# Kernel tuning notes

Measured on AMD Instinct MI355X. Metric: run time of the kernel, lower is better.

Reference implementation:

```python
import jax, jax.numpy as jnp
import numpy as np

NEG = -1e30  # stands in for -inf on the diagonal; exp(NEG - max) == 0 exactly


def setup_inputs() -> dict:
    key = jax.random.key(0)
    k1, k2, k3, k4, k5 = jax.random.split(key, 5)
    B, C, H, W = 4, 512, 128, 128
    mid = C // 8  # 64
    x = jax.random.normal(k1, (B, C, H, W), dtype=jnp.float32)
    Wq = jax.random.normal(k2, (mid, C), dtype=jnp.float32) * (1.0 / np.sqrt(C))
    Wk = jax.random.normal(k3, (mid, C), dtype=jnp.float32) * (1.0 / np.sqrt(C))
    Wv = jax.random.normal(k4, (C, C), dtype=jnp.float32) * (1.0 / np.sqrt(C))
    gamma = jax.random.normal(k5, (1,), dtype=jnp.float32) * 0.1
    return {"x": x, "Wq": Wq, "Wk": Wk, "Wv": Wv, "gamma": gamma}


def reference(x, Wq, Wk, Wv, gamma):
    B, C, H, W = x.shape
    # 1x1 convs == channel matmuls
    q = jnp.einsum('bchw,mc->bmhw', x, Wq)  # (B, mid, H, W)
    k = jnp.einsum('bchw,mc->bmhw', x, Wk)
    v = jnp.einsum('bchw,dc->bdhw', x, Wv)  # (B, C, H, W)

    # vertical (H-axis) logits with -inf diagonal: eH[b,i,w,j] = sum_m q[b,m,i,w] k[b,m,j,w]
    eH = jnp.einsum('bmiw,bmjw->biwj', q, k)           # (B, H, W, H)
    diag = jnp.eye(H, dtype=bool)[:, None, :]          # (H, 1, H)
    eH = jnp.where(diag, NEG, eH)

    # horizontal (W-axis) logits: eW[b,h,i,j] = sum_m q[b,m,h,i] k[b,m,h,j]
    eW = jnp.einsum('bmhi,bmhj->bhij', q, k)           # (B, H, W, W)

    # joint softmax over the concatenated H+W logits
    attn = jax.nn.softmax(jnp.concatenate([eH, eW], axis=3), axis=3)  # (B, H, W, H+W)
    aH = attn[:, :, :, :H]  # (B, H, W, H)
    aW = attn[:, :, :, H:]  # (B, H, W, W)

    # attention-weighted value aggregation along each axis
    outH = jnp.einsum('bcjw,biwj->bciw', v, aH)  # (B, C, H, W)
    outW = jnp.einsum('bchj,bhij->bchi', v, aW)  # (B, C, H, W)

    return gamma[0] * (outH + outW) + x
```

## Files before the change

kernel.cpp:

```cpp
#include <hip/hip_runtime.h>
#include <cstdint>
#include <cstddef>

#define NEGV (-1e30f)

constexpr int C_ = 512, H_ = 128, W_ = 128;
constexpr int P_ = 16384;

typedef short bf16x8 __attribute__((ext_vector_type(8)));
typedef float f32x4  __attribute__((ext_vector_type(4)));
typedef _Float16 f16x4 __attribute__((ext_vector_type(4)));
#define MFMA16(a, b, c) __builtin_amdgcn_mfma_f32_16x16x32_bf16((a), (b), (c), 0, 0, 0)

#define SWZ128(r, cs) (((r) << 7) + (((((cs) >> 3) ^ ((r) & 7))) << 3) + ((cs) & 7))
#define SWZ64(r, cs)  (((r) << 6) + (((((cs) >> 3) ^ ((r) & 7))) << 3) + ((cs) & 7))

__device__ inline void gl_lds16(const void* g, void* l) {
    __builtin_amdgcn_global_load_lds(
        (const __attribute__((address_space(1))) unsigned int*)g,
        (__attribute__((address_space(3))) unsigned int*)l, 16, 0, 0);
}

__device__ inline unsigned short f2bf(float f) {
    union { float f; uint32_t i; } t; t.f = f;
    uint32_t r = t.i + 0x7FFFu + ((t.i >> 16) & 1u);
    return (unsigned short)(r >> 16);
}

__global__ __launch_bounds__(256) void kwconv(
    const float* __restrict__ Wq, const float* __restrict__ Wk,
    const float* __restrict__ Wv,
    unsigned short* __restrict__ Wqkbf, unsigned short* __restrict__ Wvbf)
{
    const int i4 = (blockIdx.x * 256 + threadIdx.x) * 4;
    const float* src; unsigned short* dst; int off;
    if (i4 < 32768)       { src = Wq + i4;          dst = Wqkbf + i4; }
    else if (i4 < 65536)  { off = i4 - 32768; src = Wk + off; dst = Wqkbf + i4; }
    else                  { off = i4 - 65536; src = Wv + off; dst = Wvbf + off; }
    const float4 v = *(const float4*)src;
    ushort4 u; u.x = f2bf(v.x); u.y = f2bf(v.y); u.z = f2bf(v.z); u.w = f2bf(v.w);
    *(ushort4*)dst = u;
}

__global__ __launch_bounds__(256) void kprep1(
    const float* __restrict__ x, unsigned short* __restrict__ xTbf,
    unsigned short* __restrict__ xbf)
{
    __shared__ float t[32][33];
    const int tid = threadIdx.x;
    const int h0 = (blockIdx.x >> 2) * 32, w0 = (blockIdx.x & 3) * 32;
    const size_t base = (size_t)blockIdx.y * P_;
    {
        const int r = tid >> 3, c4 = (tid & 7) * 4;
        const float4 v = *(const float4*)&x[base + (size_t)(h0 + r) * 128 + w0 + c4];
        t[r][c4] = v.x; t[r][c4 + 1] = v.y; t[r][c4 + 2] = v.z; t[r][c4 + 3] = v.w;
        if (xbf) {
            ushort4 u; u.x = f2bf(v.x); u.y = f2bf(v.y); u.z = f2bf(v.z); u.w = f2bf(v.w);
            *(ushort4*)&xbf[base + (size_t)(h0 + r) * 128 + w0 + c4] = u;
        }
    }
    __syncthreads();
    {
        const int wr = tid >> 3, hc = (tid & 7) * 4;
        ushort4 u;
        u.x = f2bf(t[hc][wr]);     u.y = f2bf(t[hc + 1][wr]);
        u.z = f2bf(t[hc + 2][wr]); u.w = f2bf(t[hc + 3][wr]);
        *(ushort4*)&xTbf[base + (size_t)(w0 + wr) * 128 + h0 + hc] = u;
    }
}

__global__ __launch_bounds__(256) void kprep2(
    const float* __restrict__ x, unsigned short* __restrict__ xbfT)
{
    __shared__ float t[32][33];
    const int tid = threadIdx.x;
    const int p0 = blockIdx.x * 32, c0 = blockIdx.y * 32, b = blockIdx.z;
    {
        const int r = tid >> 3, c4 = (tid & 7) * 4;
        const float4 v = *(const float4*)&x[((size_t)(b * C_ + c0 + r)) * P_ + p0 + c4];
        t[r][c4] = v.x; t[r][c4 + 1] = v.y; t[r][c4 + 2] = v.z; t[r][c4 + 3] = v.w;
    }
    __syncthreads();
    {
        const int pr = tid >> 3, cc = (tid & 7) * 4;
        ushort4 u;
        u.x = f2bf(t[cc][pr]);     u.y = f2bf(t[cc + 1][pr]);
        u.z = f2bf(t[cc + 2][pr]); u.w = f2bf(t[cc + 3][pr]);
        *(ushort4*)&xbfT[((size_t)b * P_ + p0 + pr) * C_ + c0 + cc] = u;
    }
}

__global__ __launch_bounds__(256) void kgemmqk(
    const unsigned short* __restrict__ A, const unsigned short* __restrict__ Bm,
    unsigned short* __restrict__ outbf)
{
    __shared__ __attribute__((aligned(16))) unsigned short sA[2][128 * 64];
    __shared__ __attribute__((aligned(16))) unsigned short sB[2][128 * 64];
    const int tid = threadIdx.x;
    const int pbase = blockIdx.x * 128, b = blockIdx.z;
    const int lane = tid & 63, wv = tid >> 6;
    const int m0 = (wv >> 1) * 64, p0 = (wv & 1) * 64;
    const int fr = lane & 15, fq = lane >> 4;

    f32x4 acc[4][4];
#pragma unroll
    for (int i = 0; i < 4; i++)
#pragma unroll
        for (int j = 0; j < 4; j++) acc[i][j] = (f32x4){0.f, 0.f, 0.f, 0.f};

    const size_t brow0 = ((size_t)b * P_ + pbase) * 512;

#define QK_STAGE(chunk, buf) {                                                  \
        const int kc_ = (chunk) * 64;                                           \
        _Pragma("unroll")                                                       \
        for (int rep = 0; rep < 4; rep++) {                                     \
            const int idx = rep * 256 + tid;                                    \
            const int r_ = idx >> 3, kgs = (idx & 7) ^ (r_ & 7);                \
            gl_lds16(&A[(size_t)r_ * 512 + kc_ + kgs * 8], &sA[buf][idx * 8]);  \
            gl_lds16(&Bm[brow0 + (size_t)r_ * 512 + kc_ + kgs * 8], &sB[buf][idx * 8]); \
        } }

    QK_STAGE(0, 0);
    int cur = 0;
    for (int chunk = 0; chunk < 8; ++chunk) {
        if (chunk < 7) {
            QK_STAGE(chunk + 1, cur ^ 1);
            asm volatile("s_waitcnt vmcnt(8)" ::: "memory");
        } else {
            asm volatile("s_waitcnt vmcnt(0)" ::: "memory");
        }
        __builtin_amdgcn_s_barrier();
#pragma unroll
        for (int kk = 0; kk < 64; kk += 32) {
            bf16x8 af[4], bfv[4];
#pragma unroll
            for (int t = 0; t < 4; t++) af[t]  = *(const bf16x8*)&sA[cur][SWZ64(m0 + t * 16 + fr, kk + fq * 8)];
#pragma unroll
            for (int t = 0; t < 4; t++) bfv[t] = *(const bf16x8*)&sB[cur][SWZ64(p0 + t * 16 + fr, kk + fq * 8)];
#pragma unroll
            for (int i = 0; i < 4; i++)
#pragma unroll
                for (int j = 0; j < 4; j++)
                    acc[i][j] = MFMA16(af[i], bfv[j], acc[i][j]);
        }
        if (chunk < 7) __builtin_amdgcn_s_barrier();
        cur ^= 1;
    }
#undef QK_STAGE

#pragma unroll
    for (int tj = 0; tj < 4; tj++) {
        const int p_g = pbase + p0 + tj * 16 + fr;
        const size_t rowo = ((size_t)b * P_ + p_g) * 128;
#pragma unroll
        for (int ti = 0; ti < 4; ti++) {
            const int mk = m0 + ti * 16 + fq * 4;
            ushort4 u;
            u.x = f2bf(acc[ti][tj][0]); u.y = f2bf(acc[ti][tj][1]);
            u.z = f2bf(acc[ti][tj][2]); u.w = f2bf(acc[ti][tj][3]);
            *(ushort4*)&outbf[rowo + mk] = u;
        }
    }
}

__global__ __launch_bounds__(256) void klogits(
    const unsigned short* __restrict__ qkP,
    _Float16* __restrict__ ERow, _Float16* __restrict__ ECol)
{
    __shared__ __attribute__((aligned(16))) unsigned short sPM[128 * 136];
    const int tid = threadIdx.x;
    const int s = blockIdx.x, b = blockIdx.y, mode = blockIdx.z;
    const int rowMul  = mode ? 1 : 128;
    const int rowStep = mode ? 128 : 1;
    _Float16* E = mode ? ECol : ERow;
    const size_t qbase = (size_t)b * P_ * 128;
    const int rb = s * rowMul;
#pragma unroll
    for (int rep = 0; rep < 8; rep++) {
        const int idx = rep * 256 + tid;
        const int mkg = idx & 15, i = idx >> 4;
        *(uint4*)&sPM[i * 136 + mkg * 8] =
            *(const uint4*)&qkP[qbase + (size_t)(rb + i * rowStep) * 128 + mkg * 8];
    }
    __syncthreads();

    const int lane = tid & 63, wv = tid >> 6;
    const int i0 = (wv >> 1) * 64, j0 = (wv & 1) * 64;
    const int fr = lane & 15, fq = lane >> 4;

    f32x4 acc[4][4];
#pragma unroll
    for (int i = 0; i < 4; i++)
#pragma unroll
        for (int j = 0; j < 4; j++) acc[i][j] = (f32x4){0.f, 0.f, 0.f, 0.f};

#pragma unroll
    for (int kk = 0; kk < 64; kk += 32) {
        bf16x8 af[4], bfv[4];
#pragma unroll
        for (int t = 0; t < 4; t++) af[t]  = *(const bf16x8*)&sPM[(i0 + t * 16 + fr) * 136 + kk + fq * 8];
#pragma unroll
        for (int t = 0; t < 4; t++) bfv[t] = *(const bf16x8*)&sPM[(j0 + t * 16 + fr) * 136 + 64 + kk + fq * 8];
#pragma unroll
        for (int i = 0; i < 4; i++)
#pragma unroll
            for (int j = 0; j < 4; j++)
                acc[i][j] = MFMA16(af[i], bfv[j], acc[i][j]);
    }

    _Float16* Eb = E + ((size_t)(b * 128 + s)) * P_;
#pragma unroll
    for (int ti = 0; ti < 4; ti++)
#pragma unroll
        for (int r = 0; r < 4; r++) {
            const int i_g = i0 + ti * 16 + fq * 4 + r;
#pragma unroll
            for (int tj = 0; tj < 4; tj++) {
                const int j_g = j0 + tj * 16 + fr;
                float v = acc[ti][tj][r];
                if (mode && i_g == j_g) v = -60000.0f;
                Eb[(size_t)i_g * 128 + j_g] = (_Float16)v;
            }
        }
}

__global__ __launch_bounds__(256) void ksoftmax(
    const _Float16* __restrict__ ER, const _Float16* __restrict__ EC,
    unsigned short* __restrict__ AR, unsigned short* __restrict__ AC)
{
    const int tid = threadIdx.x;
    const int l32 = tid & 31;
    const int pix = blockIdx.x * 8 + (tid >> 5);
    const int b = pix >> 14, rem = pix & 16383;
    const int h = rem >> 7, w = rem & 127;
    const size_t ro = ((size_t)((b * 128 + h) * 128 + w)) * 128;
    const size_t co = ((size_t)((b * 128 + w) * 128 + h)) * 128;
    const f16x4 r = *(const f16x4*)(ER + ro + l32 * 4);
    const f16x4 c = *(const f16x4*)(EC + co + l32 * 4);
    const float r0 = r.x, r1 = r.y, r2 = r.z, r3 = r.w;
    const float c0 = c.x, c1 = c.y, c2 = c.z, c3 = c.w;
    float mx = fmaxf(fmaxf(fmaxf(r0, r1), fmaxf(r2, r3)),
                     fmaxf(fmaxf(c0, c1), fmaxf(c2, c3)));
#pragma unroll
    for (int off = 16; off > 0; off >>= 1) mx = fmaxf(mx, __shfl_xor(mx, off));
    const float e0 = __expf(r0 - mx), e1 = __expf(r1 - mx);
    const float e2 = __expf(r2 - mx), e3 = __expf(r3 - mx);
    const float f0 = __expf(c0 - mx), f1 = __expf(c1 - mx);
    const float f2 = __expf(c2 - mx), f3 = __expf(c3 - mx);
    float sm = (e0 + e1 + e2 + e3) + (f0 + f1 + f2 + f3);
#pragma unroll
    for (int off = 16; off > 0; off >>= 1) sm += __shfl_xor(sm, off);
    const float inv = 1.0f / sm;
    ushort4 u0, u1;
    u0.x = f2bf(e0 * inv); u0.y = f2bf(e1 * inv); u0.z = f2bf(e2 * inv); u0.w = f2bf(e3 * inv);
    u1.x = f2bf(f0 * inv); u1.y = f2bf(f1 * inv); u1.z = f2bf(f2 * inv); u1.w = f2bf(f3 * inv);
    *(ushort4*)(AR + ro + l32 * 4) = u0;
    *(ushort4*)(AC + co + l32 * 4) = u1;
}

__global__ __launch_bounds__(256) void kagg2(
    const unsigned short* __restrict__ ARow, const unsigned short* __restrict__ ACol,
    const float* __restrict__ x, const unsigned short* __restrict__ xbf,
    const unsigned short* __restrict__ xTbf,
    unsigned short* __restrict__ ySumR, unsigned short* __restrict__ ySumC)
{
    __shared__ __attribute__((aligned(16))) unsigned short sAttn[128 * 128];
    __shared__ __attribute__((aligned(16))) unsigned short sX[128 * 128];
    const int tid = threadIdx.x;
    const int s = blockIdx.x, b = blockIdx.y, mode = blockIdx.z;
    const int lane = tid & 63, wv = tid >> 6;
    const int m0 = (wv >> 1) * 64, n0 = (wv & 1) * 64;
    const int fr = lane & 15, fq = lane >> 4;

    const unsigned short* At = (mode ? ACol : ARow) + ((size_t)(b * 128 + s)) * P_;
#pragma unroll
    for (int rep = 0; rep < 8; rep++) {
        const int idx = rep * 256 + tid;
        const int r = idx >> 4, sl = idx & 15;
        gl_lds16(&At[(size_t)r * 128 + (sl ^ (r & 7)) * 8], &sAttn[idx * 8]);
    }

    unsigned short* yS = mode ? ySumC : ySumR;
    const unsigned short* Xsrc = mode ? xTbf : xbf;

    for (int ct = 0; ct < 4; ct++) {
        if (Xsrc) {
            const unsigned short* Xs = &Xsrc[((size_t)(b * C_ + ct * 128)) * P_ + s * 128];
#pragma unroll
            for (int rep = 0; rep < 8; rep++) {
                const int idx = rep * 256 + tid;
                const int r = idx >> 4, sl = idx & 15;
                gl_lds16(&Xs[(size_t)r * P_ + (sl ^ (r & 7)) * 8], &sX[idx * 8]);
            }
        } else {
            const float* Xf = &x[((size_t)(b * C_ + ct * 128)) * P_ + s * 128];
#pragma unroll
            for (int rep = 0; rep < 16; rep++) {
                const int idx = rep * 256 + tid;
                const int jq = idx & 31, cc = idx >> 5;
                const float4 v = *(const float4*)&Xf[(size_t)cc * P_ + jq * 4];
                ushort4 u; u.x = f2bf(v.x); u.y = f2bf(v.y); u.z = f2bf(v.z); u.w = f2bf(v.w);
                *(ushort4*)&sX[SWZ128(cc, jq * 4)] = u;
            }
        }
        __syncthreads();

        f32x4 acc[4][4];
#pragma unroll
        for (int i = 0; i < 4; i++)
#pragma unroll
            for (int j = 0; j < 4; j++) acc[i][j] = (f32x4){0.f, 0.f, 0.f, 0.f};

#pragma unroll
        for (int kk = 0; kk < 128; kk += 32) {
            bf16x8 af[4], bfv[4];
#pragma unroll
            for (int t = 0; t < 4; t++) {
                const int rc = m0 + t * 16 + fr;
                af[t] = *(const bf16x8*)&sX[SWZ128(rc, kk + fq * 8)];
            }
#pragma unroll
            for (int t = 0; t < 4; t++) {
                const int ri = n0 + t * 16 + fr;
                bfv[t] = *(const bf16x8*)&sAttn[SWZ128(ri, kk + fq * 8)];
            }
#pragma unroll
            for (int i = 0; i < 4; i++)
#pragma unroll
                for (int j = 0; j < 4; j++)
                    acc[i][j] = MFMA16(af[i], bfv[j], acc[i][j]);
        }

        const int cg0 = ct * 128 + m0 + fq * 4;
#pragma unroll
        for (int tj = 0; tj < 4; tj++) {
            const int i_g = n0 + tj * 16 + fr;
            const size_t p = mode ? ((size_t)i_g * 128 + s) : ((size_t)s * 128 + i_g);
            unsigned short* rowp = yS + ((size_t)b * P_ + p) * 512;
#pragma unroll
            for (int ti = 0; ti < 4; ti++) {
                ushort4 u;
                u.x = f2bf(acc[ti][tj][0]); u.y = f2bf(acc[ti][tj][1]);
                u.z = f2bf(acc[ti][tj][2]); u.w = f2bf(acc[ti][tj][3]);
                *(ushort4*)&rowp[cg0 + ti * 16] = u;
            }
        }
        __syncthreads();
    }
}

__global__ __launch_bounds__(512) void kfinalM(
    const unsigned short* __restrict__ Wvbf,
    const unsigned short* __restrict__ yR,
    const unsigned short* __restrict__ yC,
    float* __restrict__ outf,
    const float* __restrict__ addx,
    const float* __restrict__ gammap)
{
    __shared__ __attribute__((aligned(16))) unsigned short sM[512 * 64];
    __shared__ __attribute__((aligned(16))) unsigned short sP[128 * 64];
    const int tid = threadIdx.x;
    const int pbase = blockIdx.x * 128, b = blockIdx.z;
    const int lane = tid & 63, wv = tid >> 6;
    const int m0w = (wv >> 1) * 128;
    const int p0w = (wv & 1) * 64;
    const int fr = lane & 15, fq = lane >> 4;

    f32x4 acc[4][8];
#pragma unroll
    for (int i = 0; i < 4; i++)
#pragma unroll
        for (int j = 0; j < 8; j++) acc[i][j] = (f32x4){0.f, 0.f, 0.f, 0.f};

    const size_t brow = ((size_t)b * P_ + pbase) * 512;

    for (int hc = 0; hc < 16; ++hc) {
        const int kc = (hc >> 1) * 64;
        const unsigned short* Bsrc = (hc & 1) ? yC : yR;
        if (!(hc & 1)) {
#pragma unroll
            for (int rep = 0; rep < 8; rep++) {
                const int idx = rep * 512 + tid;
                const int r_ = idx >> 3, kgs = (idx & 7) ^ (r_ & 7);
                gl_lds16(&Wvbf[(size_t)r_ * 512 + kc + kgs * 8], &sM[idx * 8]);
            }
        }
#pragma unroll
        for (int rep = 0; rep < 2; rep++) {
            const int idx = rep * 512 + tid;
            const int r_ = idx >> 3, kgs = (idx & 7) ^ (r_ & 7);
            gl_lds16(&Bsrc[brow + (size_t)r_ * 512 + kc + kgs * 8], &sP[idx * 8]);
        }
        __syncthreads();
#pragma unroll
        for (int kk = 0; kk < 64; kk += 32) {
            bf16x8 bp[4], am[8];
#pragma unroll
            for (int t = 0; t < 4; t++) bp[t] = *(const bf16x8*)&sP[SWZ64(p0w + t * 16 + fr, kk + fq * 8)];
#pragma unroll
            for (int t = 0; t < 8; t++) am[t] = *(const bf16x8*)&sM[SWZ64(m0w + t * 16 + fr, kk + fq * 8)];
            __builtin_amdgcn_s_setprio(1);
#pragma unroll
            for (int i = 0; i < 4; i++)
#pragma unroll
                for (int j = 0; j < 8; j++)
                    acc[i][j] = MFMA16(bp[i], am[j], acc[i][j]);
            __builtin_amdgcn_s_setprio(0);
        }
        __syncthreads();
    }

    const float g = gammap[0];
#pragma unroll
    for (int ti = 0; ti < 4; ti++) {
        const int p_g = pbase + p0w + ti * 16 + fq * 4;
#pragma unroll
        for (int tj = 0; tj < 8; tj++) {
            const int m_g = m0w + tj * 16 + fr;
            const size_t off = ((size_t)(b * 512 + m_g)) * P_ + p_g;
            const float4 xa = *(const float4*)&addx[off];
            float4 o;
            o.x = fmaf(g, acc[ti][tj][0], xa.x);
            o.y = fmaf(g, acc[ti][tj][1], xa.y);
            o.z = fmaf(g, acc[ti][tj][2], xa.z);
            o.w = fmaf(g, acc[ti][tj][3], xa.w);
            *(float4*)&outf[off] = o;
        }
    }
}

extern "C" void kernel_launch(void* const* d_in, const int* in_sizes, int n_in,
                              void* d_out, int out_size, void* d_ws, size_t ws_size,
                              hipStream_t stream) {
    const float* x     = (const float*)d_in[0];
    const float* Wq    = (const float*)d_in[1];
    const float* Wk    = (const float*)d_in[2];
    const float* Wv    = (const float*)d_in[3];
    const float* gamma = (const float*)d_in[4];
    float* out = (float*)d_out;

    char* base = (char*)d_ws;
    unsigned short* Wqkbf = (unsigned short*)base;             base += 131072;
    unsigned short* Wvbf  = (unsigned short*)base;             base += 524288;
    unsigned short* xTbf  = (unsigned short*)base;             base += 67108864;
    unsigned short* xbfT  = (unsigned short*)base;             base += 67108864;
    unsigned short* qkP   = (unsigned short*)base;             base += 16777216;
    _Float16*       ERow  = (_Float16*)base;                   base += 33554432;
    _Float16*       ECol  = (_Float16*)base;                   base += 33554432;
    unsigned short* ARow  = (unsigned short*)base;             base += 16777216;
    unsigned short* ACol  = (unsigned short*)base;             base += 16777216;
    unsigned short* ySumR = (unsigned short*)base;             base += 67108864;
    unsigned short* ySumC = (unsigned short*)ERow;
    const size_t used = (size_t)(base - (char*)d_ws);
    unsigned short* xbf = nullptr;
    if (ws_size >= used + 67108864) { xbf = (unsigned short*)base; base += 67108864; }

    kwconv<<<320, 256, 0, stream>>>(Wq, Wk, Wv, Wqkbf, Wvbf);
    kprep1<<<dim3(16, 2048), 256, 0, stream>>>(x, xTbf, xbf);
    kprep2<<<dim3(512, 16, 4), 256, 0, stream>>>(x, xbfT);
    kgemmqk<<<dim3(128, 1, 4), 256, 0, stream>>>(Wqkbf, xbfT, qkP);
    klogits<<<dim3(128, 4, 2), 256, 0, stream>>>(qkP, ERow, ECol);
    ksoftmax<<<8192, 256, 0, stream>>>(ERow, ECol, ARow, ACol);
    kagg2<<<dim3(128, 4, 2), 256, 0, stream>>>(ARow, ACol, x, xbf, xTbf, ySumR, ySumC);
    kfinalM<<<dim3(128, 1, 4), 512, 0, stream>>>(Wvbf, ySumR, ySumC, out, x, gamma);
}
```

Before: 543.1 us.

## Fuse partial softmax into logits kernel and rewrite final projection GEMM

The logits kernel now computes a per-row max and sum of exponentials for each half (row and column) and writes unnormalized bf16 exponentials directly. This removes the fp16 logits round trip and the separate softmax pass. A tiny combine kernel merges the two partial statistics into per-pixel scale factors, which the aggregation kernel applies to its output. The final Wv projection is separately rewritten to read operands directly from global memory into registers without LDS, using smaller per-block tiles over more blocks. That may raise global/L2 traffic in exchange for dropping barriers and increasing occupancy.

```diff
diff --git a/kernel.cpp b/kernel.cpp
--- a/kernel.cpp
+++ b/kernel.cpp
@@ -9,7 +9,6 @@
 
 typedef short bf16x8 __attribute__((ext_vector_type(8)));
 typedef float f32x4  __attribute__((ext_vector_type(4)));
-typedef _Float16 f16x4 __attribute__((ext_vector_type(4)));
 #define MFMA16(a, b, c) __builtin_amdgcn_mfma_f32_16x16x32_bf16((a), (b), (c), 0, 0, 0)
 
 #define SWZ128(r, cs) (((r) << 7) + (((((cs) >> 3) ^ ((r) & 7))) << 3) + ((cs) & 7))
@@ -163,16 +162,21 @@
     }
 }
 
-__global__ __launch_bounds__(256) void klogits(
+__global__ __launch_bounds__(256) void klogitsP(
     const unsigned short* __restrict__ qkP,
-    _Float16* __restrict__ ERow, _Float16* __restrict__ ECol)
+    unsigned short* __restrict__ PR, unsigned short* __restrict__ PC,
+    float* __restrict__ MR, float* __restrict__ SR,
+    float* __restrict__ MC, float* __restrict__ SC)
 {
     __shared__ __attribute__((aligned(16))) unsigned short sPM[128 * 136];
+    __shared__ float red[2][128];
     const int tid = threadIdx.x;
     const int s = blockIdx.x, b = blockIdx.y, mode = blockIdx.z;
     const int rowMul  = mode ? 1 : 128;
     const int rowStep = mode ? 128 : 1;
-    _Float16* E = mode ? ECol : ERow;
+    unsigned short* PP = mode ? PC : PR;
+    float* Ma = mode ? MC : MR;
+    float* Sa = mode ? SC : SR;
     const size_t qbase = (size_t)b * P_ * 128;
     const int rb = s * rowMul;
 #pragma unroll
@@ -187,6 +191,7 @@
     const int lane = tid & 63, wv = tid >> 6;
     const int i0 = (wv >> 1) * 64, j0 = (wv & 1) * 64;
     const int fr = lane & 15, fq = lane >> 4;
+    const int jh = wv & 1;
 
     f32x4 acc[4][4];
 #pragma unroll
@@ -208,77 +213,119 @@
                 acc[i][j] = MFMA16(af[i], bfv[j], acc[i][j]);
     }
 
-    _Float16* Eb = E + ((size_t)(b * 128 + s)) * P_;
+    float mrow[4][4];
 #pragma unroll
     for (int ti = 0; ti < 4; ti++)
 #pragma unroll
         for (int r = 0; r < 4; r++) {
             const int i_g = i0 + ti * 16 + fq * 4 + r;
+            float mx = -3.0e38f;
 #pragma unroll
             for (int tj = 0; tj < 4; tj++) {
                 const int j_g = j0 + tj * 16 + fr;
                 float v = acc[ti][tj][r];
-                if (mode && i_g == j_g) v = -60000.0f;
-                Eb[(size_t)i_g * 128 + j_g] = (_Float16)v;
-            }
-        }
-}
-
-__global__ __launch_bounds__(256) void ksoftmax(
-    const _Float16* __restrict__ ER, const _Float16* __restrict__ EC,
-    unsigned short* __restrict__ AR, unsigned short* __restrict__ AC)
-{
-    const int tid = threadIdx.x;
-    const int l32 = tid & 31;
-    const int pix = blockIdx.x * 8 + (tid >> 5);
-    const int b = pix >> 14, rem = pix & 16383;
+                if (mode && i_g == j_g) v = NEGV;
+                mx = fmaxf(mx, v);
+            }
+#pragma unroll
+            for (int off = 8; off > 0; off >>= 1) mx = fmaxf(mx, __shfl_xor(mx, off));
+            red[jh][i_g] = mx;
+        }
+    __syncthreads();
+#pragma unroll
+    for (int ti = 0; ti < 4; ti++)
+#pragma unroll
+        for (int r = 0; r < 4; r++) {
+            const int i_g = i0 + ti * 16 + fq * 4 + r;
+            mrow[ti][r] = fmaxf(red[0][i_g], red[1][i_g]);
+        }
+
+    float wsum[4][4];
+    unsigned short* Pb = PP + ((size_t)(b * 128 + s)) * P_;
+#pragma unroll
+    for (int ti = 0; ti < 4; ti++)
+#pragma unroll
+        for (int r = 0; r < 4; r++) {
+            const int i_g = i0 + ti * 16 + fq * 4 + r;
+            const float m_ = mrow[ti][r];
+            float ts = 0.f;
+#pragma unroll
+            for (int tj = 0; tj < 4; tj++) {
+                const int j_g = j0 + tj * 16 + fr;
+                float v = acc[ti][tj][r];
+                if (mode && i_g == j_g) v = NEGV;
+                const float e = __expf(v - m_);
+                ts += e;
+                Pb[(size_t)i_g * 128 + j_g] = f2bf(e);
+            }
+#pragma unroll
+            for (int off = 8; off > 0; off >>= 1) ts += __shfl_xor(ts, off);
+            wsum[ti][r] = ts;
+        }
+    __syncthreads();
+#pragma unroll
+    for (int ti = 0; ti < 4; ti++)
+#pragma unroll
+        for (int r = 0; r < 4; r++)
+            red[jh][i0 + ti * 16 + fq * 4 + r] = wsum[ti][r];
+    __syncthreads();
+    if (fr == 0 && jh == 0) {
+#pragma unroll
+        for (int ti = 0; ti < 4; ti++)
+#pragma unroll
+            for (int r = 0; r < 4; r++) {
+                const int i_g = i0 + ti * 16 + fq * 4 + r;
+                const size_t o = (((size_t)b * 128 + s) << 7) + i_g;
+                Ma[o] = mrow[ti][r];
+                Sa[o] = red[0][i_g] + red[1][i_g];
+            }
+    }
+}
+
+__global__ __launch_bounds__(256) void kcomb(
+    const float* __restrict__ MR, const float* __restrict__ SR,
+    const float* __restrict__ MC, const float* __restrict__ SC,
+    float* __restrict__ FR, float* __restrict__ FC)
+{
+    const int idx = blockIdx.x * 256 + threadIdx.x;
+    const int b = idx >> 14, rem = idx & 16383;
     const int h = rem >> 7, w = rem & 127;
-    const size_t ro = ((size_t)((b * 128 + h) * 128 + w)) * 128;
-    const size_t co = ((size_t)((b * 128 + w) * 128 + h)) * 128;
-    const f16x4 r = *(const f16x4*)(ER + ro + l32 * 4);
-    const f16x4 c = *(const f16x4*)(EC + co + l32 * 4);
-    const float r0 = r.x, r1 = r.y, r2 = r.z, r3 = r.w;
-    const float c0 = c.x, c1 = c.y, c2 = c.z, c3 = c.w;
-    float mx = fmaxf(fmaxf(fmaxf(r0, r1), fmaxf(r2, r3)),
-                     fmaxf(fmaxf(c0, c1), fmaxf(c2, c3)));
-#pragma unroll
-    for (int off = 16; off > 0; off >>= 1) mx = fmaxf(mx, __shfl_xor(mx, off));
-    const float e0 = __expf(r0 - mx), e1 = __expf(r1 - mx);
-    const float e2 = __expf(r2 - mx), e3 = __expf(r3 - mx);
-    const float f0 = __expf(c0 - mx), f1 = __expf(c1 - mx);
-    const float f2 = __expf(c2 - mx), f3 = __expf(c3 - mx);
-    float sm = (e0 + e1 + e2 + e3) + (f0 + f1 + f2 + f3);
-#pragma unroll
-    for (int off = 16; off > 0; off >>= 1) sm += __shfl_xor(sm, off);
-    const float inv = 1.0f / sm;
-    ushort4 u0, u1;
-    u0.x = f2bf(e0 * inv); u0.y = f2bf(e1 * inv); u0.z = f2bf(e2 * inv); u0.w = f2bf(e3 * inv);
-    u1.x = f2bf(f0 * inv); u1.y = f2bf(f1 * inv); u1.z = f2bf(f2 * inv); u1.w = f2bf(f3 * inv);
-    *(ushort4*)(AR + ro + l32 * 4) = u0;
-    *(ushort4*)(AC + co + l32 * 4) = u1;
+    const int ro = (b << 14) + (h << 7) + w;
+    const int co = (b << 14) + (w << 7) + h;
+    const float mR = MR[ro], sR = SR[ro];
+    const float mC = MC[co], sC = SC[co];
+    const float m = fmaxf(mR, mC);
+    const float eR = __expf(mR - m), eC = __expf(mC - m);
+    const float inv = 1.0f / (sR * eR + sC * eC);
+    FR[ro] = eR * inv;
+    FC[co] = eC * inv;
 }
 
 __global__ __launch_bounds__(256) void kagg2(
-    const unsigned short* __restrict__ ARow, const unsigned short* __restrict__ ACol,
+    const unsigned short* __restrict__ PR, const unsigned short* __restrict__ PC,
     const float* __restrict__ x, const unsigned short* __restrict__ xbf,
     const unsigned short* __restrict__ xTbf,
+    const float* __restrict__ FR, const float* __restrict__ FC,
     unsigned short* __restrict__ ySumR, unsigned short* __restrict__ ySumC)
 {
     __shared__ __attribute__((aligned(16))) unsigned short sAttn[128 * 128];
     __shared__ __attribute__((aligned(16))) unsigned short sX[128 * 128];
+    __shared__ float sF[128];
     const int tid = threadIdx.x;
     const int s = blockIdx.x, b = blockIdx.y, mode = blockIdx.z;
     const int lane = tid & 63, wv = tid >> 6;
     const int m0 = (wv >> 1) * 64, n0 = (wv & 1) * 64;
     const int fr = lane & 15, fq = lane >> 4;
 
-    const unsigned short* At = (mode ? ACol : ARow) + ((size_t)(b * 128 + s)) * P_;
+    const unsigned short* At = (mode ? PC : PR) + ((size_t)(b * 128 + s)) * P_;
 #pragma unroll
     for (int rep = 0; rep < 8; rep++) {
         const int idx = rep * 256 + tid;
         const int r = idx >> 4, sl = idx & 15;
         gl_lds16(&At[(size_t)r * 128 + (sl ^ (r & 7)) * 8], &sAttn[idx * 8]);
     }
+    const float* Fsel = mode ? FC : FR;
+    if (tid < 128) sF[tid] = Fsel[(((size_t)b * 128 + s) << 7) + tid];
 
     unsigned short* yS = mode ? ySumC : ySumR;
     const unsigned short* Xsrc = mode ? xTbf : xbf;
@@ -335,13 +382,14 @@
 #pragma unroll
         for (int tj = 0; tj < 4; tj++) {
             const int i_g = n0 + tj * 16 + fr;
+            const float fsc = sF[i_g];
             const size_t p = mode ? ((size_t)i_g * 128 + s) : ((size_t)s * 128 + i_g);
             unsigned short* rowp = yS + ((size_t)b * P_ + p) * 512;
 #pragma unroll
             for (int ti = 0; ti < 4; ti++) {
                 ushort4 u;
-                u.x = f2bf(acc[ti][tj][0]); u.y = f2bf(acc[ti][tj][1]);
-                u.z = f2bf(acc[ti][tj][2]); u.w = f2bf(acc[ti][tj][3]);
+                u.x = f2bf(acc[ti][tj][0] * fsc); u.y = f2bf(acc[ti][tj][1] * fsc);
+                u.z = f2bf(acc[ti][tj][2] * fsc); u.w = f2bf(acc[ti][tj][3] * fsc);
                 *(ushort4*)&rowp[cg0 + ti * 16] = u;
             }
         }
@@ -349,7 +397,7 @@
     }
 }
 
-__global__ __launch_bounds__(512) void kfinalM(
+__global__ __launch_bounds__(256, 4) void kfinalD(
     const unsigned short* __restrict__ Wvbf,
     const unsigned short* __restrict__ yR,
     const unsigned short* __restrict__ yC,
@@ -357,66 +405,44 @@
     const float* __restrict__ addx,
     const float* __restrict__ gammap)
 {
-    __shared__ __attribute__((aligned(16))) unsigned short sM[512 * 64];
-    __shared__ __attribute__((aligned(16))) unsigned short sP[128 * 64];
-    const int tid = threadIdx.x;
-    const int pbase = blockIdx.x * 128, b = blockIdx.z;
+    const int tid = threadIdx.x;
+    const int pbase = blockIdx.x * 128, mt = blockIdx.y, b = blockIdx.z;
     const int lane = tid & 63, wv = tid >> 6;
-    const int m0w = (wv >> 1) * 128;
-    const int p0w = (wv & 1) * 64;
+    const int p0 = (wv >> 1) * 64, m0 = (wv & 1) * 64;
     const int fr = lane & 15, fq = lane >> 4;
 
-    f32x4 acc[4][8];
+    f32x4 acc[4][4];
 #pragma unroll
     for (int i = 0; i < 4; i++)
 #pragma unroll
-        for (int j = 0; j < 8; j++) acc[i][j] = (f32x4){0.f, 0.f, 0.f, 0.f};
-
-    const size_t brow = ((size_t)b * P_ + pbase) * 512;
-
-    for (int hc = 0; hc < 16; ++hc) {
-        const int kc = (hc >> 1) * 64;
-        const unsigned short* Bsrc = (hc & 1) ? yC : yR;
-        if (!(hc & 1)) {
-#pragma unroll
-            for (int rep = 0; rep < 8; rep++) {
-                const int idx = rep * 512 + tid;
-                const int r_ = idx >> 3, kgs = (idx & 7) ^ (r_ & 7);
-                gl_lds16(&Wvbf[(size_t)r_ * 512 + kc + kgs * 8], &sM[idx * 8]);
-            }
-        }
-#pragma unroll
-        for (int rep = 0; rep < 2; rep++) {
-            const int idx = rep * 512 + tid;
-            const int r_ = idx >> 3, kgs = (idx & 7) ^ (r_ & 7);
-            gl_lds16(&Bsrc[brow + (size_t)r_ * 512 + kc + kgs * 8], &sP[idx * 8]);
-        }
-        __syncthreads();
-#pragma unroll
-        for (int kk = 0; kk < 64; kk += 32) {
-            bf16x8 bp[4], am[8];
-#pragma unroll
-            for (int t = 0; t < 4; t++) bp[t] = *(const bf16x8*)&sP[SWZ64(p0w + t * 16 + fr, kk + fq * 8)];
-#pragma unroll
-            for (int t = 0; t < 8; t++) am[t] = *(const bf16x8*)&sM[SWZ64(m0w + t * 16 + fr, kk + fq * 8)];
-            __builtin_amdgcn_s_setprio(1);
+        for (int j = 0; j < 4; j++) acc[i][j] = (f32x4){0.f, 0.f, 0.f, 0.f};
+
+    const size_t aoff = ((size_t)b * P_ + pbase + p0 + fr) * 512 + fq * 8;
+    const unsigned short* bB = Wvbf + (size_t)(mt * 128 + m0 + fr) * 512 + fq * 8;
+
+    for (int half = 0; half < 2; ++half) {
+        const unsigned short* aB = (half ? yC : yR) + aoff;
+        for (int kk = 0; kk < 512; kk += 32) {
+            bf16x8 ap[4], bm[4];
+#pragma unroll
+            for (int t = 0; t < 4; t++) ap[t] = *(const bf16x8*)&aB[(size_t)(t * 16) * 512 + kk];
+#pragma unroll
+            for (int t = 0; t < 4; t++) bm[t] = *(const bf16x8*)&bB[(size_t)(t * 16) * 512 + kk];
 #pragma unroll
             for (int i = 0; i < 4; i++)
 #pragma unroll
-                for (int j = 0; j < 8; j++)
-                    acc[i][j] = MFMA16(bp[i], am[j], acc[i][j]);
-            __builtin_amdgcn_s_setprio(0);
-        }
-        __syncthreads();
+                for (int j = 0; j < 4; j++)
+                    acc[i][j] = MFMA16(ap[i], bm[j], acc[i][j]);
+        }
     }
 
     const float g = gammap[0];
 #pragma unroll
     for (int ti = 0; ti < 4; ti++) {
-        const int p_g = pbase + p0w + ti * 16 + fq * 4;
-#pragma unroll
-        for (int tj = 0; tj < 8; tj++) {
-            const int m_g = m0w + tj * 16 + fr;
+        const int p_g = pbase + p0 + ti * 16 + fq * 4;
+#pragma unroll
+        for (int tj = 0; tj < 4; tj++) {
+            const int m_g = mt * 128 + m0 + tj * 16 + fr;
             const size_t off = ((size_t)(b * 512 + m_g)) * P_ + p_g;
             const float4 xa = *(const float4*)&addx[off];
             float4 o;
@@ -445,12 +471,17 @@
     unsigned short* xTbf  = (unsigned short*)base;             base += 67108864;
     unsigned short* xbfT  = (unsigned short*)base;             base += 67108864;
     unsigned short* qkP   = (unsigned short*)base;             base += 16777216;
-    _Float16*       ERow  = (_Float16*)base;                   base += 33554432;
-    _Float16*       ECol  = (_Float16*)base;                   base += 33554432;
-    unsigned short* ARow  = (unsigned short*)base;             base += 16777216;
-    unsigned short* ACol  = (unsigned short*)base;             base += 16777216;
+    char*           freeRC = base;                             base += 67108864;
+    unsigned short* PR    = (unsigned short*)base;             base += 16777216;
+    unsigned short* PC    = (unsigned short*)base;             base += 16777216;
     unsigned short* ySumR = (unsigned short*)base;             base += 67108864;
-    unsigned short* ySumC = (unsigned short*)ERow;
+    float*          MR    = (float*)base;                      base += 262144;
+    float*          SR    = (float*)base;                      base += 262144;
+    float*          MC    = (float*)base;                      base += 262144;
+    float*          SC    = (float*)base;                      base += 262144;
+    float*          FR    = (float*)base;                      base += 262144;
+    float*          FC    = (float*)base;                      base += 262144;
+    unsigned short* ySumC = (unsigned short*)freeRC;
     const size_t used = (size_t)(base - (char*)d_ws);
     unsigned short* xbf = nullptr;
     if (ws_size >= used + 67108864) { xbf = (unsigned short*)base; base += 67108864; }
@@ -459,8 +490,8 @@
     kprep1<<<dim3(16, 2048), 256, 0, stream>>>(x, xTbf, xbf);
     kprep2<<<dim3(512, 16, 4), 256, 0, stream>>>(x, xbfT);
     kgemmqk<<<dim3(128, 1, 4), 256, 0, stream>>>(Wqkbf, xbfT, qkP);
-    klogits<<<dim3(128, 4, 2), 256, 0, stream>>>(qkP, ERow, ECol);
-    ksoftmax<<<8192, 256, 0, stream>>>(ERow, ECol, ARow, ACol);
-    kagg2<<<dim3(128, 4, 2), 256, 0, stream>>>(ARow, ACol, x, xbf, xTbf, ySumR, ySumC);
-    kfinalM<<<dim3(128, 1, 4), 512, 0, stream>>>(Wvbf, ySumR, ySumC, out, x, gamma);
-}
+    klogitsP<<<dim3(128, 4, 2), 256, 0, stream>>>(qkP, PR, PC, MR, SR, MC, SC);
+    kcomb<<<256, 256, 0, stream>>>(MR, SR, MC, SC, FR, FC);
+    kagg2<<<dim3(128, 4, 2), 256, 0, stream>>>(PR, PC, x, xbf, xTbf, FR, FC, ySumR, ySumC);
+    kfinalD<<<dim3(128, 4, 4), 256, 0, stream>>>(Wvbf, ySumR, ySumC, out, x, gamma);
+}
```

Result: slower. 874.0 us (+60.9%).
